# Performance work log

Measured on AMD Instinct MI355X. Metric: run time of the kernel, lower is better.

Reference implementation:

```python
import jax, jax.numpy as jnp
import numpy as np

MAX_POS = float(2 ** 20)  # max_position_encoding_distance
B, C, S = 2, 1536, 16384
H, T, P = 768, 367, 128
NUM_ORG = 2


def _apply_rope(x, positions):
    # x: (B, P, T, H), positions: (B, P) int -> rotate pairs (first-half, second-half)
    half = x.shape[-1] // 2
    inv_freq = 1.0 / (MAX_POS ** (jnp.arange(half, dtype=jnp.float32) / half))  # (half,)
    ang = positions.astype(jnp.float32)[:, :, None, None] * inv_freq  # (B, P, 1, half)
    cos, sin = jnp.cos(ang), jnp.sin(ang)
    x1, x2 = x[..., :half], x[..., half:]
    return jnp.concatenate([x1 * cos - x2 * sin, x1 * sin + x2 * cos], axis=-1)


def _gather_affine_rope(logits, idx, params, organism_index):
    # logits: (B, H, S); idx: (B, P); params: (ORG, 2, T, H)
    bi = jnp.arange(logits.shape[0])[:, None]
    x = logits[bi, :, idx]  # (B, P, H)
    bp = params[organism_index]  # (B, 2, T, H)
    scale = bp[:, 0][:, None]   # (B, 1, T, H)
    offset = bp[:, 1][:, None]  # (B, 1, T, H)
    x = scale * x[:, :, None, :] + offset  # (B, P, T, H)
    return _apply_rope(x, idx)


def setup_inputs() -> dict:
    key = jax.random.key(0)
    ks = jax.random.split(key, 9)
    stdv = 1.0 / np.sqrt(C)
    return {
        'embeddings_1bp': jax.random.normal(ks[0], (B, C, S), jnp.float32),
        'conv_w': jax.random.normal(ks[1], (NUM_ORG, H, C), jnp.float32) * stdv,
        'conv_b': jax.random.normal(ks[2], (NUM_ORG, H), jnp.float32) * 0.02,
        'rope_pos_donor': jax.random.normal(ks[3], (NUM_ORG, 2, T, H), jnp.float32) * 0.05,
        'rope_pos_acceptor': jax.random.normal(ks[4], (NUM_ORG, 2, T, H), jnp.float32) * 0.05,
        'rope_neg_donor': jax.random.normal(ks[5], (NUM_ORG, 2, T, H), jnp.float32) * 0.05,
        'rope_neg_acceptor': jax.random.normal(ks[6], (NUM_ORG, 2, T, H), jnp.float32) * 0.05,
        'organism_index': jax.random.randint(ks[7], (B,), 0, NUM_ORG),
        'splice_site_positions': jax.random.randint(ks[8], (B, 4, P), 0, S),
    }


def reference(embeddings_1bp, conv_w, conv_b, rope_pos_donor, rope_pos_acceptor,
              rope_neg_donor, rope_neg_acceptor, organism_index, splice_site_positions):
    pos_d, pos_a = splice_site_positions[:, 0], splice_site_positions[:, 1]
    neg_d, neg_a = splice_site_positions[:, 2], splice_site_positions[:, 3]

    # organism-indexed 1x1 conv: (B,C,S) x (B,H,C) -> (B,H,S)
    w = conv_w[organism_index]
    b = conv_b[organism_index]
    logits = jnp.einsum('bcs,boc->bos', embeddings_1bp, w) + b[:, :, None]

    pdl = _gather_affine_rope(logits, pos_d, rope_pos_donor, organism_index)
    pal = _gather_affine_rope(logits, pos_a, rope_pos_acceptor, organism_index)
    ndl = _gather_affine_rope(logits, neg_d, rope_neg_donor, organism_index)
    nal = _gather_affine_rope(logits, neg_a, rope_neg_acceptor, organism_index)

    pos_counts = jax.nn.softplus(jnp.einsum('bdth,bath->bdat', pdl, pal))  # (B,P,P,T)
    neg_counts = jax.nn.softplus(jnp.einsum('bdth,bath->bdat', ndl, nal))

    pos_mask = (pos_d >= 0)[:, :, None] & (pos_a >= 0)[:, None, :]  # (B,P,P)
    neg_mask = (neg_d >= 0)[:, :, None] & (neg_a >= 0)[:, None, :]
    # tissue_mask: default num_tracks_per_organism -> all True
    tissue_mask = jnp.ones((B, T), dtype=bool)
    pos_mask = pos_mask[:, :, :, None] & tissue_mask[:, None, None, :]
    neg_mask = neg_mask[:, :, :, None] & tissue_mask[:, None, None, :]

    junction_mask = jnp.concatenate([pos_mask, neg_mask], axis=-1)  # (B,P,P,2T)
    pred_counts = jnp.concatenate([pos_counts, neg_counts], axis=-1)
    pred_counts = jnp.where(junction_mask, pred_counts, 0.0)
    return pred_counts, junction_mask
```

## Files before the change

kernel.cpp:

```cpp
#include <hip/hip_runtime.h>
#include <hip/hip_bf16.h>
#include <math.h>
#include <string.h>

#define B_    2
#define C_    1536
#define S_    16384
#define H_    768
#define T_    367
#define P_    128
#define HALF_ 384
#define TT_   734
#define PRED_ELEMS 24051712

#define XHH_OFF  0
#define CSH_OFF  393216
#define INVF_OFF 786432
#define XCB_OFF  787200

typedef short short8 __attribute__((ext_vector_type(8)));
typedef _Float16 f16x8 __attribute__((ext_vector_type(8)));
typedef _Float16 h2    __attribute__((ext_vector_type(2)));
typedef float f32x4  __attribute__((ext_vector_type(4)));

__device__ __forceinline__ unsigned int packbf2(float a, float b) {
    __hip_bfloat162 h = __float22bfloat162_rn(make_float2(a, b));
    unsigned int r; __builtin_memcpy(&r, &h, 4); return r;
}
__device__ __forceinline__ unsigned short packbf1(float a) {
    __hip_bfloat16 h = __float2bfloat16(a);
    unsigned short r; __builtin_memcpy(&r, &h, 2); return r;
}
__device__ __forceinline__ unsigned short f2h(float x) {
    _Float16 h = (_Float16)x;
    unsigned short r; __builtin_memcpy(&r, &h, 2); return r;
}
__device__ __forceinline__ h2 bch(unsigned int v) { h2 r; __builtin_memcpy(&r, &v, 4); return r; }
__device__ __forceinline__ unsigned int hcb(h2 v) { unsigned int r; __builtin_memcpy(&r, &v, 4); return r; }

__global__ void gather_cols(const float* __restrict__ emb,
                            const int* __restrict__ sp,
                            unsigned short* __restrict__ xcb) {
    int blk = blockIdx.x;
    int p = blk & 127;
    int g = (blk >> 7) & 3;
    int b = blk >> 9;
    int s = sp[(b * 4 + g) * P_ + p];
    const float* src = emb + (size_t)b * C_ * S_ + s;
    unsigned short* dst = xcb + ((size_t)(b * 4 + g) * P_ + p) * C_;
    for (int c = threadIdx.x; c < C_; c += blockDim.x)
        dst[c] = packbf1(src[(size_t)c * S_]);
}

__global__ __launch_bounds__(256) void logits_mfma(
    const unsigned short* __restrict__ xcb, const float* __restrict__ w,
    const float* __restrict__ bias, const int* __restrict__ org,
    unsigned short* __restrict__ xhh) {
    __shared__ __align__(16) unsigned short tX[64 * 64];
    __shared__ __align__(16) unsigned short tW[64 * 64];
    int mt = blockIdx.x;
    int nt = blockIdx.y;
    int o = org[mt >> 3];
    int r0 = mt * 64, h0 = nt * 64;
    int tid = threadIdx.x;
    int lane = tid & 63, wid = tid >> 6;
    int wrow = (wid >> 1) * 32, wcol = (wid & 1) * 32;
    int lr = lane & 15, lq = lane >> 4;
    int gr0 = (lq ^ (lr & 7)) * 8;

    f32x4 acc[2][2];
    #pragma unroll
    for (int i = 0; i < 2; ++i)
        #pragma unroll
        for (int j = 0; j < 2; ++j) acc[i][j] = (f32x4){0.f, 0.f, 0.f, 0.f};

    int srow = tid >> 2, sg = tid & 3;

    for (int kc = 0; kc < C_; kc += 64) {
        if (kc) __syncthreads();
        {
            const unsigned short* src = xcb + (size_t)(r0 + srow) * C_ + kc;
            unsigned short* drow = tX + srow * 64;
            #pragma unroll
            for (int i = 0; i < 2; ++i) {
                int g = sg + i * 4;
                uint4 v = *(const uint4*)(src + g * 8);
                *(uint4*)&drow[(g ^ (srow & 7)) * 8] = v;
            }
        }
        {
            const float* srcw = w + ((size_t)o * H_ + h0 + srow) * C_ + kc;
            unsigned short* drow = tW + srow * 64;
            #pragma unroll
            for (int i = 0; i < 2; ++i) {
                int g = sg + i * 4;
                float4 v0 = *(const float4*)(srcw + g * 8);
                float4 v1 = *(const float4*)(srcw + g * 8 + 4);
                uint4 pk;
                pk.x = packbf2(v0.x, v0.y); pk.y = packbf2(v0.z, v0.w);
                pk.z = packbf2(v1.x, v1.y); pk.w = packbf2(v1.z, v1.w);
                *(uint4*)&drow[(g ^ (srow & 7)) * 8] = pk;
            }
        }
        __syncthreads();
        #pragma unroll
        for (int kk = 0; kk < 64; kk += 32) {
            short8 af[2], bf2[2];
            #pragma unroll
            for (int fi = 0; fi < 2; ++fi)
                af[fi] = *(const short8*)&tX[(wrow + fi * 16 + lr) * 64 + (gr0 ^ kk)];
            #pragma unroll
            for (int fj = 0; fj < 2; ++fj)
                bf2[fj] = *(const short8*)&tW[(wcol + fj * 16 + lr) * 64 + (gr0 ^ kk)];
            #pragma unroll
            for (int fi = 0; fi < 2; ++fi)
                #pragma unroll
                for (int fj = 0; fj < 2; ++fj)
                    acc[fi][fj] = __builtin_amdgcn_mfma_f32_16x16x32_bf16(
                        af[fi], bf2[fj], acc[fi][fj], 0, 0, 0);
        }
    }
    #pragma unroll
    for (int fi = 0; fi < 2; ++fi)
        #pragma unroll
        for (int rr = 0; rr < 4; ++rr) {
            int r = r0 + wrow + fi * 16 + lq * 4 + rr;
            #pragma unroll
            for (int fj = 0; fj < 2; ++fj) {
                int h = h0 + wcol + fj * 16 + lr;
                int hj = (h < HALF_) ? h : (h - HALF_);
                int sel = (h < HALF_) ? 0 : 1;
                xhh[(size_t)r * H_ + (hj >> 2) * 8 + sel * 4 + (hj & 3)] =
                    f2h(acc[fi][fj][rr] + bias[o * H_ + h]);
            }
        }
}

__global__ void init_invf(double* __restrict__ invf) {
    int j = threadIdx.x;
    if (j < HALF_) invf[j] = exp2(-20.0 * (double)j / 384.0);
}

__global__ void rope_table(const int* __restrict__ sp,
                           const double* __restrict__ invf,
                           unsigned short* __restrict__ csh) {
    int e = blockIdx.x * blockDim.x + threadIdx.x;
    if (e >= B_ * 4 * P_ * HALF_) return;
    int j = e % HALF_;
    int r = e / HALF_;
    int s = sp[r];
    const double TWO_PI = 6.283185307179586476925286766559;
    double ang = (double)s * invf[j];
    double k = rint(ang * (1.0 / TWO_PI));
    float fr = (float)(ang - k * TWO_PI);
    float sv, cv;
    __sincosf(fr, &sv, &cv);
    int base = r * H_ + (j >> 2) * 8 + (j & 3);
    csh[base]     = f2h(cv);
    csh[base + 4] = f2h(sv);
}

__global__ __launch_bounds__(512, 4) void junction_mfma(
    const unsigned short* __restrict__ xhh, const unsigned short* __restrict__ csh,
    const float* __restrict__ rpd, const float* __restrict__ rpa,
    const float* __restrict__ rnd, const float* __restrict__ rna,
    const int* __restrict__ org, const int* __restrict__ sp,
    unsigned short* __restrict__ w1) {
    __shared__ __align__(16) unsigned short smem[32768];
    __shared__ __align__(16) unsigned short scofh[4 * H_];
    __shared__ int vD[P_], vA[P_];

    int nwg = gridDim.x;
    int orig = blockIdx.x;
    int xcd = orig & 7;
    int q = nwg >> 3, r8 = nwg & 7;
    int blk = (xcd < r8 ? xcd * (q + 1) : r8 * (q + 1) + (xcd - r8) * q) + (orig >> 3);

    int t = blk % T_;
    int sign = (blk / T_) & 1;
    int b = blk / (2 * T_);
    int o = org[b];
    int gd = sign * 2, ga = sign * 2 + 1;
    const float* pd = sign ? rnd : rpd;
    const float* pa = sign ? rna : rpa;
    int tid = threadIdx.x;

    const float* sc_d = pd + ((size_t)(o * 2 + 0) * T_ + t) * H_;
    const float* of_d = pd + ((size_t)(o * 2 + 1) * T_ + t) * H_;
    const float* sc_a = pa + ((size_t)(o * 2 + 0) * T_ + t) * H_;
    const float* of_a = pa + ((size_t)(o * 2 + 1) * T_ + t) * H_;
    for (int e = tid; e < H_; e += 512) {
        int hj = (e < HALF_) ? e : (e - HALF_);
        int pos = (hj >> 2) * 8 + ((e < HALF_) ? 0 : 4) + (hj & 3);
        scofh[pos]           = f2h(sc_d[e]);
        scofh[H_ + pos]      = f2h(of_d[e]);
        scofh[2 * H_ + pos]  = f2h(sc_a[e]);
        scofh[3 * H_ + pos]  = f2h(of_a[e]);
    }
    if (tid < P_) {
        vD[tid] = sp[(b * 4 + gd) * P_ + tid] >= 0;
        vA[tid] = sp[(b * 4 + ga) * P_ + tid] >= 0;
    }
    const unsigned short* xdh = xhh + ((size_t)(b * 4 + gd) * P_) * H_;
    const unsigned short* xah = xhh + ((size_t)(b * 4 + ga) * P_) * H_;
    const unsigned short* cdh = csh + ((size_t)(b * 4 + gd) * P_) * H_;
    const unsigned short* cah = csh + ((size_t)(b * 4 + ga) * P_) * H_;

    int lane = tid & 63, wid = tid >> 6;
    int wrow = (wid >> 2) * 64, wcol = (wid & 3) * 32;
    int lr = lane & 15, lq = lane >> 4;
    int gr0 = (lq ^ (lr & 7)) * 8;

    f32x4 acc[4][2];
    #pragma unroll
    for (int i = 0; i < 4; ++i)
        #pragma unroll
        for (int j = 0; j < 2; ++j) acc[i][j] = (f32x4){0.f, 0.f, 0.f, 0.f};

    int jp = tid & 7;
    int prow = tid >> 3;
    int swc = ((jp ^ (prow & 7)) << 3);

    __syncthreads();

    for (int ch = 0; ch < 12; ++ch) {
        int kb = (ch * 8 + jp) * 8;
        unsigned short* tDc = smem + (ch & 1) * 16384;
        unsigned short* tAc = tDc + 8192;

        uint4 scd = *(const uint4*)&scofh[kb];
        uint4 ofd = *(const uint4*)&scofh[H_ + kb];
        uint4 sca = *(const uint4*)&scofh[2 * H_ + kb];
        uint4 ofa = *(const uint4*)&scofh[3 * H_ + kb];

        #pragma unroll
        for (int pass = 0; pass < 2; ++pass) {
            int p = pass * 64 + prow;
            int sw = p * 64 + swc;
            {
                uint4 xv = *(const uint4*)(xdh + p * H_ + kb);
                uint4 cv = *(const uint4*)(cdh + p * H_ + kb);
                h2 u1a = __builtin_elementwise_fma(bch(scd.x), bch(xv.x), bch(ofd.x));
                h2 u1b = __builtin_elementwise_fma(bch(scd.y), bch(xv.y), bch(ofd.y));
                h2 u2a = __builtin_elementwise_fma(bch(scd.z), bch(xv.z), bch(ofd.z));
                h2 u2b = __builtin_elementwise_fma(bch(scd.w), bch(xv.w), bch(ofd.w));
                h2 cA = bch(cv.x), cB = bch(cv.y), sA = bch(cv.z), sB = bch(cv.w);
                h2 r1a = __builtin_elementwise_fma(u1a, cA, -(u2a * sA));
                h2 r1b = __builtin_elementwise_fma(u1b, cB, -(u2b * sB));
                h2 r2a = __builtin_elementwise_fma(u1a, sA, u2a * cA);
                h2 r2b = __builtin_elementwise_fma(u1b, sB, u2b * cB);
                uint4 wv;
                wv.x = hcb(r1a); wv.y = hcb(r1b); wv.z = hcb(r2a); wv.w = hcb(r2b);
                *(uint4*)&tDc[sw] = wv;
            }
            {
                uint4 xv = *(const uint4*)(xah + p * H_ + kb);
                uint4 cv = *(const uint4*)(cah + p * H_ + kb);
                h2 u1a = __builtin_elementwise_fma(bch(sca.x), bch(xv.x), bch(ofa.x));
                h2 u1b = __builtin_elementwise_fma(bch(sca.y), bch(xv.y), bch(ofa.y));
                h2 u2a = __builtin_elementwise_fma(bch(sca.z), bch(xv.z), bch(ofa.z));
                h2 u2b = __builtin_elementwise_fma(bch(sca.w), bch(xv.w), bch(ofa.w));
                h2 cA = bch(cv.x), cB = bch(cv.y), sA = bch(cv.z), sB = bch(cv.w);
                h2 r1a = __builtin_elementwise_fma(u1a, cA, -(u2a * sA));
                h2 r1b = __builtin_elementwise_fma(u1b, cB, -(u2b * sB));
                h2 r2a = __builtin_elementwise_fma(u1a, sA, u2a * cA);
                h2 r2b = __builtin_elementwise_fma(u1b, sB, u2b * cB);
                uint4 wv;
                wv.x = hcb(r1a); wv.y = hcb(r1b); wv.z = hcb(r2a); wv.w = hcb(r2b);
                *(uint4*)&tAc[sw] = wv;
            }
        }
        __syncthreads();

        __builtin_amdgcn_s_setprio(1);
        #pragma unroll
        for (int kk = 0; kk < 64; kk += 32) {
            f16x8 af[4], bf2[2];
            #pragma unroll
            for (int fi = 0; fi < 4; ++fi)
                af[fi] = *(const f16x8*)&tDc[(wrow + fi * 16 + lr) * 64 + (gr0 ^ kk)];
            #pragma unroll
            for (int fj = 0; fj < 2; ++fj)
                bf2[fj] = *(const f16x8*)&tAc[(wcol + fj * 16 + lr) * 64 + (gr0 ^ kk)];
            #pragma unroll
            for (int fi = 0; fi < 4; ++fi)
                #pragma unroll
                for (int fj = 0; fj < 2; ++fj)
                    acc[fi][fj] = __builtin_amdgcn_mfma_f32_16x16x32_f16(
                        af[fi], bf2[fj], acc[fi][fj], 0, 0, 0);
        }
        __builtin_amdgcn_s_setprio(0);
    }

    #pragma unroll
    for (int fi = 0; fi < 4; ++fi) {
        #pragma unroll
        for (int rr = 0; rr < 4; ++rr) {
            int d = wrow + fi * 16 + lq * 4 + rr;
            int vd = vD[d];
            #pragma unroll
            for (int fj = 0; fj < 2; ++fj) {
                int a = wcol + fj * 16 + lr;
                float x = acc[fi][fj][rr];
                float v = 0.0f;
                if (vd && vA[a]) v = (x > 15.0f) ? x : __logf(1.0f + __expf(x));
                smem[d * P_ + a] = packbf1(v);
            }
        }
    }
    __syncthreads();
    const uint4* src4 = (const uint4*)smem;
    uint4* dst4 = (uint4*)(w1 + ((size_t)((b * 2 + sign) * T_ + t) * P_) * P_);
    for (int i = tid; i < 2048; i += 512) dst4[i] = src4[i];
}

__global__ __launch_bounds__(256) void transpose_out(const __hip_bfloat16* __restrict__ w1,
                                                     float* __restrict__ pred) {
    __shared__ float tile[64 * 129];
    int blk = blockIdx.x;
    int tt = blk % 6;
    int d = (blk / 6) % P_;
    int bs = blk / (6 * P_);
    int b = bs >> 1, sign = bs & 1;
    int t0 = tt * 64;
    int tcnt = min(64, T_ - t0);
    int tid = threadIdx.x;

    const __hip_bfloat16* src = w1 + (size_t)bs * T_ * P_ * P_ + (size_t)d * P_;
    for (int e = tid; e < tcnt * P_; e += 256) {
        int i = e >> 7, a = e & 127;
        tile[i * 129 + a] = __bfloat162float(src[(size_t)(t0 + i) * P_ * P_ + a]);
    }
    __syncthreads();
    float* dst = pred + ((size_t)(b * P_ + d) * P_) * TT_ + sign * T_ + t0;
    for (int e = tid; e < P_ * 64; e += 256) {
        int a = e >> 6, ii = e & 63;
        if (ii < tcnt) dst[(size_t)a * TT_ + ii] = tile[ii * 129 + a];
    }
}

__global__ void mask_fill(const int* __restrict__ sp, float* __restrict__ mask) {
    int blk = blockIdx.x;
    int a = blk & 127;
    int d = (blk >> 7) & 127;
    int b = blk >> 14;
    bool vp = (sp[(b * 4 + 0) * P_ + d] >= 0) && (sp[(b * 4 + 1) * P_ + a] >= 0);
    bool vn = (sp[(b * 4 + 2) * P_ + d] >= 0) && (sp[(b * 4 + 3) * P_ + a] >= 0);
    float* dst = mask + (size_t)blk * TT_;
    for (int st = threadIdx.x; st < TT_; st += blockDim.x)
        dst[st] = (st < T_ ? vp : vn) ? 1.0f : 0.0f;
}

extern "C" void kernel_launch(void* const* d_in, const int* in_sizes, int n_in,
                              void* d_out, int out_size, void* d_ws, size_t ws_size,
                              hipStream_t stream) {
    const float* emb  = (const float*)d_in[0];
    const float* w    = (const float*)d_in[1];
    const float* bias = (const float*)d_in[2];
    const float* rpd  = (const float*)d_in[3];
    const float* rpa  = (const float*)d_in[4];
    const float* rnd  = (const float*)d_in[5];
    const float* rna  = (const float*)d_in[6];
    const int*   org  = (const int*)d_in[7];
    const int*   sp   = (const int*)d_in[8];

    float* out = (float*)d_out;
    float* ws  = (float*)d_ws;
    unsigned short* xhh = (unsigned short*)(ws + XHH_OFF);
    unsigned short* csh = (unsigned short*)(ws + CSH_OFF);
    double* invf = (double*)(ws + INVF_OFF);
    unsigned short* xcb = (unsigned short*)(ws + XCB_OFF);
    float* pred  = out;
    float* maskp = out + PRED_ELEMS;
    unsigned short* w1 = (unsigned short*)maskp;

    init_invf<<<1, 384, 0, stream>>>(invf);
    gather_cols<<<1024, 256, 0, stream>>>(emb, sp, xcb);
    rope_table<<<1536, 256, 0, stream>>>(sp, invf, csh);
    dim3 gl(16, 12);
    logits_mfma<<<gl, 256, 0, stream>>>(xcb, w, bias, org, xhh);
    junction_mfma<<<2 * 2 * T_, 512, 0, stream>>>(xhh, csh, rpd, rpa, rnd, rna, org, sp, w1);
    transpose_out<<<2 * 2 * P_ * 6, 256, 0, stream>>>((const __hip_bfloat16*)w1, pred);
    mask_fill<<<32768, 256, 0, stream>>>(sp, maskp);
}
```

Before: 217.4 us.

## Process two tissue tracks per junction block to share gathered logits and rope loads

```diff
diff --git a/kernel.cpp b/kernel.cpp
--- a/kernel.cpp
+++ b/kernel.cpp
@@ -11,6 +11,7 @@
 #define P_    128
 #define HALF_ 384
 #define TT_   734
+#define NT2_  184
 #define PRED_ELEMS 24051712
 
 #define XHH_OFF  0
@@ -160,14 +161,14 @@
     csh[base + 4] = f2h(sv);
 }
 
-__global__ __launch_bounds__(512, 4) void junction_mfma(
+__global__ __launch_bounds__(1024, 4) void junction_mfma(
     const unsigned short* __restrict__ xhh, const unsigned short* __restrict__ csh,
     const float* __restrict__ rpd, const float* __restrict__ rpa,
     const float* __restrict__ rnd, const float* __restrict__ rna,
     const int* __restrict__ org, const int* __restrict__ sp,
     unsigned short* __restrict__ w1) {
-    __shared__ __align__(16) unsigned short smem[32768];
-    __shared__ __align__(16) unsigned short scofh[4 * H_];
+    __shared__ __align__(16) unsigned short smem[65536];
+    __shared__ __align__(16) unsigned short scofh[6144];
     __shared__ int vD[P_], vA[P_];
 
     int nwg = gridDim.x;
@@ -176,26 +177,31 @@
     int q = nwg >> 3, r8 = nwg & 7;
     int blk = (xcd < r8 ? xcd * (q + 1) : r8 * (q + 1) + (xcd - r8) * q) + (orig >> 3);
 
-    int t = blk % T_;
-    int sign = (blk / T_) & 1;
-    int b = blk / (2 * T_);
+    int tp = blk % NT2_;
+    int sign = (blk / NT2_) & 1;
+    int b = blk / (2 * NT2_);
     int o = org[b];
+    int t0 = 2 * tp, t1 = t0 + 1;
+    int t1ok = (t1 < T_);
+    int t1c = t1ok ? t1 : t0;
     int gd = sign * 2, ga = sign * 2 + 1;
     const float* pd = sign ? rnd : rpd;
     const float* pa = sign ? rna : rpa;
     int tid = threadIdx.x;
 
-    const float* sc_d = pd + ((size_t)(o * 2 + 0) * T_ + t) * H_;
-    const float* of_d = pd + ((size_t)(o * 2 + 1) * T_ + t) * H_;
-    const float* sc_a = pa + ((size_t)(o * 2 + 0) * T_ + t) * H_;
-    const float* of_a = pa + ((size_t)(o * 2 + 1) * T_ + t) * H_;
-    for (int e = tid; e < H_; e += 512) {
-        int hj = (e < HALF_) ? e : (e - HALF_);
-        int pos = (hj >> 2) * 8 + ((e < HALF_) ? 0 : 4) + (hj & 3);
-        scofh[pos]           = f2h(sc_d[e]);
-        scofh[H_ + pos]      = f2h(of_d[e]);
-        scofh[2 * H_ + pos]  = f2h(sc_a[e]);
-        scofh[3 * H_ + pos]  = f2h(of_a[e]);
+    for (int e = tid; e < 6144; e += 1024) {
+        int tsel = e / 3072;
+        int rem = e - tsel * 3072;
+        int side = rem / 1536;
+        int rem2 = rem - side * 1536;
+        int arr = rem2 / 768;
+        int e2 = rem2 - arr * 768;
+        int tt = tsel ? t1c : t0;
+        const float* base = (side ? pa : pd) + ((size_t)(o * 2 + arr) * T_ + tt) * H_;
+        int hj = (e2 < HALF_) ? e2 : (e2 - HALF_);
+        int sel = (e2 < HALF_) ? 0 : 1;
+        int pos = (hj >> 2) * 8 + sel * 4 + (hj & 3);
+        scofh[((tsel * 2 + side) * 2 + arr) * 768 + pos] = f2h(base[e2]);
     }
     if (tid < P_) {
         vD[tid] = sp[(b * 4 + gd) * P_ + tid] >= 0;
@@ -207,93 +213,116 @@
     const unsigned short* cah = csh + ((size_t)(b * 4 + ga) * P_) * H_;
 
     int lane = tid & 63, wid = tid >> 6;
-    int wrow = (wid >> 2) * 64, wcol = (wid & 3) * 32;
+    int wrow = (wid >> 2) * 32, wcol = (wid & 3) * 32;
     int lr = lane & 15, lq = lane >> 4;
     int gr0 = (lq ^ (lr & 7)) * 8;
 
-    f32x4 acc[4][2];
+    f32x4 a0[2][2], a1[2][2];
     #pragma unroll
-    for (int i = 0; i < 4; ++i)
-        #pragma unroll
-        for (int j = 0; j < 2; ++j) acc[i][j] = (f32x4){0.f, 0.f, 0.f, 0.f};
-
-    int jp = tid & 7;
-    int prow = tid >> 3;
-    int swc = ((jp ^ (prow & 7)) << 3);
+    for (int i = 0; i < 2; ++i)
+        #pragma unroll
+        for (int j = 0; j < 2; ++j) {
+            a0[i][j] = (f32x4){0.f, 0.f, 0.f, 0.f};
+            a1[i][j] = (f32x4){0.f, 0.f, 0.f, 0.f};
+        }
 
     __syncthreads();
 
     for (int ch = 0; ch < 12; ++ch) {
-        int kb = (ch * 8 + jp) * 8;
-        unsigned short* tDc = smem + (ch & 1) * 16384;
-        unsigned short* tAc = tDc + 8192;
-
-        uint4 scd = *(const uint4*)&scofh[kb];
-        uint4 ofd = *(const uint4*)&scofh[H_ + kb];
-        uint4 sca = *(const uint4*)&scofh[2 * H_ + kb];
-        uint4 ofa = *(const uint4*)&scofh[3 * H_ + kb];
-
-        #pragma unroll
-        for (int pass = 0; pass < 2; ++pass) {
-            int p = pass * 64 + prow;
-            int sw = p * 64 + swc;
+        unsigned short* bufb = smem + (ch & 1) * 32768;
+
+        #pragma unroll
+        for (int s = 0; s < 2; ++s) {
+            int slot = tid + s * 1024;
+            int row = slot >> 3, gran = slot & 7;
+            int side = row >> 7, prow = row & 127;
+            const unsigned short* xb = side ? xah : xdh;
+            const unsigned short* cb = side ? cah : cdh;
+            int off = prow * H_ + ch * 64 + gran * 8;
+            uint4 xv = *(const uint4*)(xb + off);
+            uint4 cv = *(const uint4*)(cb + off);
+            int sw = prow * 64 + ((gran ^ (prow & 7)) << 3);
+            int kb = (ch * 8 + gran) * 8;
+            h2 cA = bch(cv.x), cB = bch(cv.y), sA = bch(cv.z), sB = bch(cv.w);
             {
-                uint4 xv = *(const uint4*)(xdh + p * H_ + kb);
-                uint4 cv = *(const uint4*)(cdh + p * H_ + kb);
-                h2 u1a = __builtin_elementwise_fma(bch(scd.x), bch(xv.x), bch(ofd.x));
-                h2 u1b = __builtin_elementwise_fma(bch(scd.y), bch(xv.y), bch(ofd.y));
-                h2 u2a = __builtin_elementwise_fma(bch(scd.z), bch(xv.z), bch(ofd.z));
-                h2 u2b = __builtin_elementwise_fma(bch(scd.w), bch(xv.w), bch(ofd.w));
-                h2 cA = bch(cv.x), cB = bch(cv.y), sA = bch(cv.z), sB = bch(cv.w);
-                h2 r1a = __builtin_elementwise_fma(u1a, cA, -(u2a * sA));
-                h2 r1b = __builtin_elementwise_fma(u1b, cB, -(u2b * sB));
-                h2 r2a = __builtin_elementwise_fma(u1a, sA, u2a * cA);
-                h2 r2b = __builtin_elementwise_fma(u1b, sB, u2b * cB);
+                const unsigned short* cof = scofh + (side * 2) * 768;
+                uint4 sc = *(const uint4*)(cof + kb);
+                uint4 of = *(const uint4*)(cof + 768 + kb);
+                h2 u1a = __builtin_elementwise_fma(bch(sc.x), bch(xv.x), bch(of.x));
+                h2 u1b = __builtin_elementwise_fma(bch(sc.y), bch(xv.y), bch(of.y));
+                h2 u2a = __builtin_elementwise_fma(bch(sc.z), bch(xv.z), bch(of.z));
+                h2 u2b = __builtin_elementwise_fma(bch(sc.w), bch(xv.w), bch(of.w));
                 uint4 wv;
-                wv.x = hcb(r1a); wv.y = hcb(r1b); wv.z = hcb(r2a); wv.w = hcb(r2b);
-                *(uint4*)&tDc[sw] = wv;
+                wv.x = hcb(__builtin_elementwise_fma(u1a, cA, -(u2a * sA)));
+                wv.y = hcb(__builtin_elementwise_fma(u1b, cB, -(u2b * sB)));
+                wv.z = hcb(__builtin_elementwise_fma(u1a, sA, u2a * cA));
+                wv.w = hcb(__builtin_elementwise_fma(u1b, sB, u2b * cB));
+                *(uint4*)&bufb[side * 8192 + sw] = wv;
             }
             {
-                uint4 xv = *(const uint4*)(xah + p * H_ + kb);
-                uint4 cv = *(const uint4*)(cah + p * H_ + kb);
-                h2 u1a = __builtin_elementwise_fma(bch(sca.x), bch(xv.x), bch(ofa.x));
-                h2 u1b = __builtin_elementwise_fma(bch(sca.y), bch(xv.y), bch(ofa.y));
-                h2 u2a = __builtin_elementwise_fma(bch(sca.z), bch(xv.z), bch(ofa.z));
-                h2 u2b = __builtin_elementwise_fma(bch(sca.w), bch(xv.w), bch(ofa.w));
-                h2 cA = bch(cv.x), cB = bch(cv.y), sA = bch(cv.z), sB = bch(cv.w);
-                h2 r1a = __builtin_elementwise_fma(u1a, cA, -(u2a * sA));
-                h2 r1b = __builtin_elementwise_fma(u1b, cB, -(u2b * sB));
-                h2 r2a = __builtin_elementwise_fma(u1a, sA, u2a * cA);
-                h2 r2b = __builtin_elementwise_fma(u1b, sB, u2b * cB);
+                const unsigned short* cof = scofh + ((2 + side) * 2) * 768;
+                uint4 sc = *(const uint4*)(cof + kb);
+                uint4 of = *(const uint4*)(cof + 768 + kb);
+                h2 u1a = __builtin_elementwise_fma(bch(sc.x), bch(xv.x), bch(of.x));
+                h2 u1b = __builtin_elementwise_fma(bch(sc.y), bch(xv.y), bch(of.y));
+                h2 u2a = __builtin_elementwise_fma(bch(sc.z), bch(xv.z), bch(of.z));
+                h2 u2b = __builtin_elementwise_fma(bch(sc.w), bch(xv.w), bch(of.w));
                 uint4 wv;
-                wv.x = hcb(r1a); wv.y = hcb(r1b); wv.z = hcb(r2a); wv.w = hcb(r2b);
-                *(uint4*)&tAc[sw] = wv;
+                wv.x = hcb(__builtin_elementwise_fma(u1a, cA, -(u2a * sA)));
+                wv.y = hcb(__builtin_elementwise_fma(u1b, cB, -(u2b * sB)));
+                wv.z = hcb(__builtin_elementwise_fma(u1a, sA, u2a * cA));
+                wv.w = hcb(__builtin_elementwise_fma(u1b, sB, u2b * cB));
+                *(uint4*)&bufb[16384 + side * 8192 + sw] = wv;
             }
         }
         __syncthreads();
 
         __builtin_amdgcn_s_setprio(1);
-        #pragma unroll
-        for (int kk = 0; kk < 64; kk += 32) {
-            f16x8 af[4], bf2[2];
-            #pragma unroll
-            for (int fi = 0; fi < 4; ++fi)
-                af[fi] = *(const f16x8*)&tDc[(wrow + fi * 16 + lr) * 64 + (gr0 ^ kk)];
-            #pragma unroll
-            for (int fj = 0; fj < 2; ++fj)
-                bf2[fj] = *(const f16x8*)&tAc[(wcol + fj * 16 + lr) * 64 + (gr0 ^ kk)];
-            #pragma unroll
-            for (int fi = 0; fi < 4; ++fi)
+        {
+            const unsigned short* tD = bufb;
+            const unsigned short* tA = bufb + 8192;
+            #pragma unroll
+            for (int kk = 0; kk < 64; kk += 32) {
+                f16x8 af[2], bf2[2];
+                #pragma unroll
+                for (int fi = 0; fi < 2; ++fi)
+                    af[fi] = *(const f16x8*)&tD[(wrow + fi * 16 + lr) * 64 + (gr0 ^ kk)];
                 #pragma unroll
                 for (int fj = 0; fj < 2; ++fj)
-                    acc[fi][fj] = __builtin_amdgcn_mfma_f32_16x16x32_f16(
-                        af[fi], bf2[fj], acc[fi][fj], 0, 0, 0);
+                    bf2[fj] = *(const f16x8*)&tA[(wcol + fj * 16 + lr) * 64 + (gr0 ^ kk)];
+                #pragma unroll
+                for (int fi = 0; fi < 2; ++fi)
+                    #pragma unroll
+                    for (int fj = 0; fj < 2; ++fj)
+                        a0[fi][fj] = __builtin_amdgcn_mfma_f32_16x16x32_f16(
+                            af[fi], bf2[fj], a0[fi][fj], 0, 0, 0);
+            }
+        }
+        {
+            const unsigned short* tD = bufb + 16384;
+            const unsigned short* tA = bufb + 24576;
+            #pragma unroll
+            for (int kk = 0; kk < 64; kk += 32) {
+                f16x8 af[2], bf2[2];
+                #pragma unroll
+                for (int fi = 0; fi < 2; ++fi)
+                    af[fi] = *(const f16x8*)&tD[(wrow + fi * 16 + lr) * 64 + (gr0 ^ kk)];
+                #pragma unroll
+                for (int fj = 0; fj < 2; ++fj)
+                    bf2[fj] = *(const f16x8*)&tA[(wcol + fj * 16 + lr) * 64 + (gr0 ^ kk)];
+                #pragma unroll
+                for (int fi = 0; fi < 2; ++fi)
+                    #pragma unroll
+                    for (int fj = 0; fj < 2; ++fj)
+                        a1[fi][fj] = __builtin_amdgcn_mfma_f32_16x16x32_f16(
+                            af[fi], bf2[fj], a1[fi][fj], 0, 0, 0);
+            }
         }
         __builtin_amdgcn_s_setprio(0);
     }
 
     #pragma unroll
-    for (int fi = 0; fi < 4; ++fi) {
+    for (int fi = 0; fi < 2; ++fi) {
         #pragma unroll
         for (int rr = 0; rr < 4; ++rr) {
             int d = wrow + fi * 16 + lq * 4 + rr;
@@ -301,17 +330,26 @@
             #pragma unroll
             for (int fj = 0; fj < 2; ++fj) {
                 int a = wcol + fj * 16 + lr;
-                float x = acc[fi][fj][rr];
-                float v = 0.0f;
-                if (vd && vA[a]) v = (x > 15.0f) ? x : __logf(1.0f + __expf(x));
-                smem[d * P_ + a] = packbf1(v);
+                int va = vA[a];
+                float x0 = a0[fi][fj][rr];
+                float v0 = 0.0f;
+                if (vd && va) v0 = (x0 > 15.0f) ? x0 : __logf(1.0f + __expf(x0));
+                smem[d * P_ + a] = packbf1(v0);
+                float x1 = a1[fi][fj][rr];
+                float v1 = 0.0f;
+                if (vd && va) v1 = (x1 > 15.0f) ? x1 : __logf(1.0f + __expf(x1));
+                smem[16384 + d * P_ + a] = packbf1(v1);
             }
         }
     }
     __syncthreads();
-    const uint4* src4 = (const uint4*)smem;
-    uint4* dst4 = (uint4*)(w1 + ((size_t)((b * 2 + sign) * T_ + t) * P_) * P_);
-    for (int i = tid; i < 2048; i += 512) dst4[i] = src4[i];
+    const uint4* s4 = (const uint4*)smem;
+    uint4* d40 = (uint4*)(w1 + (size_t)((b * 2 + sign) * T_ + t0) * (P_ * P_));
+    for (int i = tid; i < 2048; i += 1024) d40[i] = s4[i];
+    if (t1ok) {
+        uint4* d41 = (uint4*)(w1 + (size_t)((b * 2 + sign) * T_ + t1) * (P_ * P_));
+        for (int i = tid; i < 2048; i += 1024) d41[i] = s4[2048 + i];
+    }
 }
 
 __global__ __launch_bounds__(256) void transpose_out(const __hip_bfloat16* __restrict__ w1,
@@ -379,7 +417,7 @@
     rope_table<<<1536, 256, 0, stream>>>(sp, invf, csh);
     dim3 gl(16, 12);
     logits_mfma<<<gl, 256, 0, stream>>>(xcb, w, bias, org, xhh);
-    junction_mfma<<<2 * 2 * T_, 512, 0, stream>>>(xhh, csh, rpd, rpa, rnd, rna, org, sp, w1);
+    junction_mfma<<<2 * 2 * NT2_, 1024, 0, stream>>>(xhh, csh, rpd, rpa, rnd, rna, org, sp, w1);
     transpose_out<<<2 * 2 * P_ * 6, 256, 0, stream>>>((const __hip_bfloat16*)w1, pred);
     mask_fill<<<32768, 256, 0, stream>>>(sp, maskp);
 }
```

After: 214.5 us. No clear change (-1.3%).
